# Performance work log

Hardware: AMD Instinct MI355X
Metric: run time of the kernel (lower is better)

Reference implementation:

```python
import jax, jax.numpy as jnp
import numpy as np

DILATION = (1, 1)


def pd_indexing2d(x, dh, dw, dilation):
    """Pitch-dependent indexing. x:(B,C,H,W); dh,dw:(B,1,W) -> list of 9 (B,C,H,W)."""
    B, C, H, W = x.shape
    # dilation factors, clamped to >= 1, broadcast to (B,1,1,W)
    dil_h = jnp.maximum((dh * dilation[0]).astype(jnp.int32), 1)[:, :, None, :]
    dil_w = jnp.maximum((dw * dilation[1]).astype(jnp.int32), 1)[:, :, None, :]

    rH = jnp.arange(H)[None, None, :, None]   # (1,1,H,1)
    cW = jnp.arange(W)[None, None, None, :]   # (1,1,1,W)

    # row (frequency) indices
    idxD = jnp.abs(rH - dil_h) % H            # (B,1,H,W)
    up = rH + dil_h
    idxU = jnp.where(up >= H, rH, up)         # overflow -> idxU - dil = base
    rows = [idxD, jnp.broadcast_to(rH, (1, 1, H, 1)), idxU]

    # col (time) indices
    idxL = jnp.abs(cW - dil_w) % W            # (B,1,1,W)
    rt = cW + dil_w
    # torch uses negative index -(rt % W) - 1 == W - 1 - (rt % W)
    idxR = jnp.where(rt >= W, W - 1 - (rt % W), rt)
    cols = [idxL, jnp.broadcast_to(cW, (1, 1, 1, W)), idxR]

    bidx = jnp.arange(B).reshape(B, 1, 1, 1)
    cidx = jnp.arange(C).reshape(1, C, 1, 1)
    xs = []
    for r in rows:
        for c in cols:
            xs.append(x[bidx, cidx, r, c])
    return xs


def setup_inputs() -> dict:
    key = jax.random.key(0)
    k1, k2, k3, k4, k5 = jax.random.split(key, 5)
    B, C, O, H, W = 8, 64, 64, 80, 800
    x = jax.random.normal(k1, (B, C, H, W), dtype=jnp.float32)
    dh = jax.random.randint(k2, (B, 1, W), 1, 4).astype(jnp.float32)
    dw = jax.random.randint(k3, (B, 1, W), 1, 4).astype(jnp.float32)
    weight = jax.random.normal(k4, (9, O, C), dtype=jnp.float32) * 0.05
    bias = jax.random.normal(k5, (O,), dtype=jnp.float32) * 0.05
    return {"x": x, "dh": dh, "dw": dw, "weight": weight, "bias": bias}


def reference(x, dh, dw, weight, bias):
    xs = pd_indexing2d(x, dh, dw, DILATION)
    out = jnp.einsum('bchw,oc->bohw', xs[0], weight[0]) + bias[None, :, None, None]
    for k in range(1, 9):
        out = out + jnp.einsum('bchw,oc->bohw', xs[k], weight[k])
    return out
```

## Files before the change

### kernel.cpp

```cpp
#include <hip/hip_runtime.h>

#define B_  8
#define C_  64
#define O_  64
#define H_  80
#define W_  800
#define NCHUNK 13
#define XT_BYTES 65536000u

typedef short bf16x8 __attribute__((ext_vector_type(8)));
typedef float f32x4  __attribute__((ext_vector_type(4)));

__device__ __forceinline__ unsigned short f2bf(float f) {
    unsigned int u = __float_as_uint(f);
    unsigned int r = u + 0x7FFFu + ((u >> 16) & 1u);
    return (unsigned short)(r >> 16);
}

__global__ void k_transpose(const float* __restrict__ x, unsigned short* __restrict__ xT) {
    __shared__ float tile[64][65];
    const int chunk = blockIdx.x, h = blockIdx.y, b = blockIdx.z;
    const int w0 = chunk * 64;
    const int tid = threadIdx.x;

    const int w = tid & 63, c0 = tid >> 6;
#pragma unroll
    for (int it = 0; it < 16; ++it) {
        const int c = it * 4 + c0;
        float v = 0.f;
        if (w0 + w < W_) v = x[(((b * C_ + c) * H_ + h) * W_) + w0 + w];
        tile[c][w] = v;
    }
    __syncthreads();

    const int cp = tid & 31;
    const int wr = tid >> 5;
#pragma unroll
    for (int it = 0; it < 8; ++it) {
        const int ww = it * 8 + wr;
        if (w0 + ww < W_) {
            unsigned int lo = (unsigned int)f2bf(tile[2 * cp][ww]);
            unsigned int hi = (unsigned int)f2bf(tile[2 * cp + 1][ww]);
            ((unsigned int*)xT)[(((b * H_ + h) * W_) + w0 + ww) * 32 + cp] = lo | (hi << 16);
        }
    }
}

__global__ void k_wfrag(const float* __restrict__ wt, unsigned short* __restrict__ wf) {
    const int t = blockIdx.x * 256 + threadIdx.x;
    const int j    = t & 7;
    const int lane = (t >> 3) & 63;
    const int mt   = (t >> 9) & 3;
    const int ks   = t >> 11;
    const int tap  = ks >> 1, hf = ks & 1;
    const int o = mt * 16 + (lane & 15);
    const int c = hf * 32 + (lane >> 4) * 8 + j;
    wf[t] = f2bf(wt[(tap * 64 + o) * 64 + c]);
}

__global__ void k_main(const unsigned short* __restrict__ xT,
                       const unsigned short* __restrict__ wfrag,
                       const float* __restrict__ dh, const float* __restrict__ dw,
                       const float* __restrict__ bias, float* __restrict__ out) {
    const int tid  = threadIdx.x;
    const int wave = tid >> 6, lane = tid & 63;
    const int chunk = blockIdx.x;
    const int h = blockIdx.y * 4 + wave;
    const int b = blockIdx.z;
    const int w0 = chunk * 64;
    const int l15 = lane & 15, kq = lane >> 4;

    unsigned int ro[4][3], co[4][3];
#pragma unroll
    for (int nt = 0; nt < 4; ++nt) {
        const int pw  = w0 + nt * 16 + l15;
        const int pwc = pw < W_ ? pw : W_ - 1;
        const int dhi = (int)dh[b * W_ + pwc];
        const int dwi = (int)dw[b * W_ + pwc];
        int rD = h - dhi;   if (rD < 0) rD = -rD;
        const int rU = (h + dhi < H_) ? (h + dhi) : h;
        int cL = pwc - dwi; if (cL < 0) cL = -cL;
        const int cR = (pwc + dwi < W_) ? (pwc + dwi) : (2 * W_ - 1 - pwc - dwi);
        ro[nt][0] = (unsigned int)(b * H_ + rD) * 102400u;
        ro[nt][1] = (unsigned int)(b * H_ + h ) * 102400u;
        ro[nt][2] = (unsigned int)(b * H_ + rU) * 102400u;
        co[nt][0] = (unsigned int)cL  * 128u;
        co[nt][1] = (unsigned int)pwc * 128u;
        co[nt][2] = (unsigned int)cR  * 128u;
    }

    const char* xTb = (const char*)xT;
    const char* wfb = (const char*)wfrag;
    const unsigned int aoff = (unsigned int)lane * 16u;
    const unsigned int boff = (unsigned int)kq * 16u;

    f32x4 acc[4][4];
#pragma unroll
    for (int mt = 0; mt < 4; ++mt) {
        const f32x4 bv = *(const f32x4*)(bias + mt * 16 + kq * 4);
#pragma unroll
        for (int nt = 0; nt < 4; ++nt)
#pragma unroll
            for (int r = 0; r < 4; ++r) acc[mt][nt][r] = bv[r];
    }

#pragma unroll
    for (int tap = 0; tap < 9; ++tap) {
        const int i = tap / 3, j = tap % 3;
#pragma unroll
        for (int hf = 0; hf < 2; ++hf) {
            bf16x8 bfr[4], afr[4];
#pragma unroll
            for (int nt = 0; nt < 4; ++nt)
                bfr[nt] = *(const bf16x8*)(xTb + (ro[nt][i] + co[nt][j]
                                                 + (unsigned int)(hf * 64) + boff));
#pragma unroll
            for (int mt = 0; mt < 4; ++mt)
                afr[mt] = *(const bf16x8*)(wfb
                           + (unsigned int)(((tap * 2 + hf) * 4 + mt) * 1024) + aoff);
#pragma unroll
            for (int mt = 0; mt < 4; ++mt)
#pragma unroll
                for (int nt = 0; nt < 4; ++nt)
                    acc[mt][nt] = __builtin_amdgcn_mfma_f32_16x16x32_bf16(
                        afr[mt], bfr[nt], acc[mt][nt], 0, 0, 0);
        }
    }

#pragma unroll
    for (int mt = 0; mt < 4; ++mt) {
#pragma unroll
        for (int nt = 0; nt < 4; ++nt) {
            const int w = w0 + nt * 16 + l15;
            if (w < W_) {
                const unsigned int ob =
                    ((unsigned int)(b * O_ + mt * 16 + kq * 4) * (unsigned int)H_
                     + (unsigned int)h) * (unsigned int)W_ + (unsigned int)w;
#pragma unroll
                for (int r = 0; r < 4; ++r)
                    out[ob + (unsigned int)r * 64000u] = acc[mt][nt][r];
            }
        }
    }
}

extern "C" void kernel_launch(void* const* d_in, const int* in_sizes, int n_in,
                              void* d_out, int out_size, void* d_ws, size_t ws_size,
                              hipStream_t stream) {
    const float* x      = (const float*)d_in[0];
    const float* dh     = (const float*)d_in[1];
    const float* dw     = (const float*)d_in[2];
    const float* weight = (const float*)d_in[3];
    const float* bias   = (const float*)d_in[4];
    float* out = (float*)d_out;

    unsigned short* xT    = (unsigned short*)d_ws;
    unsigned short* wfrag = (unsigned short*)((char*)d_ws + XT_BYTES);

    k_transpose<<<dim3(NCHUNK, H_, B_), 256, 0, stream>>>(x, xT);
    k_wfrag<<<dim3(144), 256, 0, stream>>>(weight, wfrag);
    k_main<<<dim3(NCHUNK, H_ / 4, B_), 256, 0, stream>>>(xT, wfrag, dh, dw, bias, out);
}
```

Before: 347.9 us.

## Vectorize transpose and software-pipeline operand loads in main MFMA loop

The transpose kernel now reads float4 vectors and writes 32-byte packed bf16 chunks per pixel instead of scalar accesses. The main kernel double-buffers A and B fragments in registers so the next tap's global loads are issued before the current MFMAs. It also adds launch bounds targeting three blocks per SIMD group and flattens the grid so batch varies fastest across consecutive blocks. Extra fragment registers may raise pressure, and the launch bounds could force spills.

```diff
diff --git a/kernel.cpp b/kernel.cpp
--- a/kernel.cpp
+++ b/kernel.cpp
@@ -18,31 +18,36 @@
 }
 
 __global__ void k_transpose(const float* __restrict__ x, unsigned short* __restrict__ xT) {
-    __shared__ float tile[64][65];
+    __shared__ float tile[64][68];
     const int chunk = blockIdx.x, h = blockIdx.y, b = blockIdx.z;
     const int w0 = chunk * 64;
     const int tid = threadIdx.x;
 
-    const int w = tid & 63, c0 = tid >> 6;
+    const int wf4 = tid & 15;
+    const int c0  = tid >> 4;
+    const int w   = w0 + wf4 * 4;
 #pragma unroll
-    for (int it = 0; it < 16; ++it) {
-        const int c = it * 4 + c0;
-        float v = 0.f;
-        if (w0 + w < W_) v = x[(((b * C_ + c) * H_ + h) * W_) + w0 + w];
-        tile[c][w] = v;
+    for (int it = 0; it < 4; ++it) {
+        const int c = it * 16 + c0;
+        f32x4 v = {0.f, 0.f, 0.f, 0.f};
+        if (w < W_) v = *(const f32x4*)(x + (((b * C_ + c) * H_ + h) * W_) + w);
+        *(f32x4*)&tile[c][wf4 * 4] = v;
     }
     __syncthreads();
 
-    const int cp = tid & 31;
-    const int wr = tid >> 5;
+    const int px = tid >> 2, q = tid & 3;
+    if (w0 + px < W_) {
+        unsigned int u[8];
 #pragma unroll
-    for (int it = 0; it < 8; ++it) {
-        const int ww = it * 8 + wr;
-        if (w0 + ww < W_) {
-            unsigned int lo = (unsigned int)f2bf(tile[2 * cp][ww]);
-            unsigned int hi = (unsigned int)f2bf(tile[2 * cp + 1][ww]);
-            ((unsigned int*)xT)[(((b * H_ + h) * W_) + w0 + ww) * 32 + cp] = lo | (hi << 16);
+        for (int i = 0; i < 8; ++i) {
+            const int c = q * 16 + 2 * i;
+            u[i] = (unsigned int)f2bf(tile[c][px])
+                 | ((unsigned int)f2bf(tile[c + 1][px]) << 16);
         }
+        unsigned int* dst = (unsigned int*)xT
+            + ((size_t)((b * H_ + h) * W_) + w0 + px) * 32 + q * 8;
+        *(uint4*)(dst)     = make_uint4(u[0], u[1], u[2], u[3]);
+        *(uint4*)(dst + 4) = make_uint4(u[4], u[5], u[6], u[7]);
     }
 }
 
@@ -58,15 +63,20 @@
     wf[t] = f2bf(wt[(tap * 64 + o) * 64 + c]);
 }
 
-__global__ void k_main(const unsigned short* __restrict__ xT,
-                       const unsigned short* __restrict__ wfrag,
-                       const float* __restrict__ dh, const float* __restrict__ dw,
-                       const float* __restrict__ bias, float* __restrict__ out) {
+__global__ void __launch_bounds__(256, 3)
+k_main(const unsigned short* __restrict__ xT,
+       const unsigned short* __restrict__ wfrag,
+       const float* __restrict__ dh, const float* __restrict__ dw,
+       const float* __restrict__ bias, float* __restrict__ out) {
     const int tid  = threadIdx.x;
     const int wave = tid >> 6, lane = tid & 63;
-    const int chunk = blockIdx.x;
-    const int h = blockIdx.y * 4 + wave;
-    const int b = blockIdx.z;
+
+    const unsigned int flat = blockIdx.x;
+    const int b     = flat & 7;
+    const unsigned int l = flat >> 3;
+    const int chunk = l % NCHUNK;
+    const int by    = l / NCHUNK;
+    const int h  = by * 4 + wave;
     const int w0 = chunk * 64;
     const int l15 = lane & 15, kq = lane >> 4;
 
@@ -104,26 +114,40 @@
             for (int r = 0; r < 4; ++r) acc[mt][nt][r] = bv[r];
     }
 
+    bf16x8 bcur[4], acur[4], bnxt[4], anxt[4];
 #pragma unroll
-    for (int tap = 0; tap < 9; ++tap) {
-        const int i = tap / 3, j = tap % 3;
+    for (int nt = 0; nt < 4; ++nt)
+        bcur[nt] = *(const bf16x8*)(xTb + (ro[nt][0] + co[nt][0] + boff));
 #pragma unroll
-        for (int hf = 0; hf < 2; ++hf) {
-            bf16x8 bfr[4], afr[4];
+    for (int mt = 0; mt < 4; ++mt)
+        acur[mt] = *(const bf16x8*)(wfb + (unsigned int)(mt * 1024) + aoff);
+
+#pragma unroll
+    for (int s = 0; s < 18; ++s) {
+        if (s < 17) {
+            const int sn = s + 1;
+            const int tap = sn >> 1, hf = sn & 1;
+            const int i = tap / 3, j = tap % 3;
 #pragma unroll
             for (int nt = 0; nt < 4; ++nt)
-                bfr[nt] = *(const bf16x8*)(xTb + (ro[nt][i] + co[nt][j]
-                                                 + (unsigned int)(hf * 64) + boff));
+                bnxt[nt] = *(const bf16x8*)(xTb + (ro[nt][i] + co[nt][j]
+                                                  + (unsigned int)(hf * 64) + boff));
 #pragma unroll
             for (int mt = 0; mt < 4; ++mt)
-                afr[mt] = *(const bf16x8*)(wfb
-                           + (unsigned int)(((tap * 2 + hf) * 4 + mt) * 1024) + aoff);
+                anxt[mt] = *(const bf16x8*)(wfb
+                             + (unsigned int)((sn * 4 + mt) * 1024) + aoff);
+        }
 #pragma unroll
-            for (int mt = 0; mt < 4; ++mt)
+        for (int mt = 0; mt < 4; ++mt)
 #pragma unroll
-                for (int nt = 0; nt < 4; ++nt)
-                    acc[mt][nt] = __builtin_amdgcn_mfma_f32_16x16x32_bf16(
-                        afr[mt], bfr[nt], acc[mt][nt], 0, 0, 0);
+            for (int nt = 0; nt < 4; ++nt)
+                acc[mt][nt] = __builtin_amdgcn_mfma_f32_16x16x32_bf16(
+                    acur[mt], bcur[nt], acc[mt][nt], 0, 0, 0);
+        if (s < 17) {
+#pragma unroll
+            for (int nt = 0; nt < 4; ++nt) bcur[nt] = bnxt[nt];
+#pragma unroll
+            for (int mt = 0; mt < 4; ++mt) acur[mt] = anxt[mt];
         }
     }
 
@@ -159,5 +183,5 @@
 
     k_transpose<<<dim3(NCHUNK, H_, B_), 256, 0, stream>>>(x, xT);
     k_wfrag<<<dim3(144), 256, 0, stream>>>(weight, wfrag);
-    k_main<<<dim3(NCHUNK, H_ / 4, B_), 256, 0, stream>>>(xT, wfrag, dh, dw, bias, out);
+    k_main<<<dim3(NCHUNK * (H_ / 4) * B_), 256, 0, stream>>>(xT, wfrag, dh, dw, bias, out);
 }
```

New measurement: 332.5 us. -4.4%, faster.
